# Kernel tuning notes

Hardware: AMD Instinct MI355X
Metric: run time of the kernel (lower is better)

The kernel has to match this reference:

```python
import jax, jax.numpy as jnp
import numpy as np

B, N, D, P_IN, P_OUT = 8, 2048, 32, 8, 4


def setup_inputs() -> dict:
    key = jax.random.key(0)
    k1, k2, k3, k4 = jax.random.split(key, 4)
    U = jax.random.normal(k1, (B, N, D, P_IN), dtype=jnp.float32)
    A = jax.random.uniform(k2, (B, N, N), dtype=jnp.float32)
    W_self = jax.random.normal(k3, (P_IN, P_OUT), dtype=jnp.float32) * 0.01
    W_neigh = jax.random.normal(k4, (P_IN, P_OUT), dtype=jnp.float32) * 0.01
    bias = jnp.zeros((1, 1, 1, P_OUT), dtype=jnp.float32)
    return {"U": U, "A": A, "W_self": W_self, "W_neigh": W_neigh, "bias": bias}


def _stiefel_projection(Y_flat):
    # Polar factor: Y = W S V^T  ->  proj = W V^T (same as Y @ (Y^T Y)^{-1/2})
    u, _, vt = jnp.linalg.svd(Y_flat, full_matrices=False)
    return u @ vt


def reference(U, A, W_self, W_neigh, bias):
    # U: (B,N,d,p_in); A: (B,N,N)
    M_self = jnp.einsum('bndi,io->bndo', U, W_self)
    M_neigh = jnp.einsum('bndi,io->bndo', U, W_neigh)
    # dense neighborhood aggregation: A @ reshape(M_neigh, (B,N,d*p_out))
    M_agg = jnp.einsum('bnm,bmdo->bndo', A, M_neigh)
    Y = jax.nn.relu(M_self + M_agg + bias)
    Y_flat = Y.reshape(B * N, D, P_OUT)
    U_proj = _stiefel_projection(Y_flat)
    return U_proj.reshape(B, N, D, P_OUT)
```

## Files before the change

kernel.cpp:

```cpp
#include <hip/hip_runtime.h>
#include <math.h>

constexpr int B_   = 8;
constexpr int N_   = 2048;
constexpr int D_   = 32;
constexpr int PIN  = 8;
constexpr int POUT = 4;
constexpr int COLS = 128;
constexpr int BM   = 32;
constexpr int BK   = 64;
constexpr int NT   = N_ / BK;

using f32x4  = __attribute__((ext_vector_type(4))) float;
using bf16x8 = __attribute__((ext_vector_type(8))) short;

__device__ __forceinline__ unsigned short f2bf(float f) {
    union { float f; unsigned u; } v; v.f = f;
    unsigned u = v.u + 0x7fffu + ((v.u >> 16) & 1u);
    return (unsigned short)(u >> 16);
}

__global__ __launch_bounds__(256) void mneigh_t_kernel(
    const float* __restrict__ U, const float* __restrict__ Wn,
    unsigned short* __restrict__ Btg)
{
    const int bt = blockIdx.x;
    const int b  = bt >> 5;
    const int n0 = (bt & 31) * 64;
    const int t  = threadIdx.x;
    const int d  = t >> 3;
    const int ns = t & 7;

    float w[PIN][POUT];
#pragma unroll
    for (int p = 0; p < PIN; ++p)
#pragma unroll
        for (int o = 0; o < POUT; ++o) w[p][o] = Wn[p * POUT + o];

    union { unsigned short s[8]; int4 v; } ob[POUT];
    const float* Ub = U + (((size_t)(b * N_ + n0 + ns * 8)) * D_ + d) * PIN;
#pragma unroll
    for (int ni = 0; ni < 8; ++ni) {
        const float4 u0 = *(const float4*)(Ub + (size_t)ni * D_ * PIN);
        const float4 u1 = *(const float4*)(Ub + (size_t)ni * D_ * PIN + 4);
        const float uu[8] = {u0.x, u0.y, u0.z, u0.w, u1.x, u1.y, u1.z, u1.w};
#pragma unroll
        for (int o = 0; o < POUT; ++o) {
            float s = 0.f;
#pragma unroll
            for (int p = 0; p < PIN; ++p) s = fmaf(uu[p], w[p][o], s);
            ob[o].s[ni] = f2bf(s);
        }
    }
#pragma unroll
    for (int o = 0; o < POUT; ++o) {
        unsigned short* dst =
            Btg + ((size_t)(b * COLS + d * 4 + o)) * N_ + n0 + ns * 8;
        *(int4*)dst = ob[o].v;
    }
}

__global__ __launch_bounds__(512) void gemm_proj_kernel(
    const float* __restrict__ A, const unsigned short* __restrict__ Btg,
    const float* __restrict__ U, const float* __restrict__ Wsg,
    const float* __restrict__ bias, float* __restrict__ out)
{
    __shared__ unsigned char smem[40960];
    float* Yl = (float*)smem;
    float* Gp = (float*)(smem + 16896);
    float* Sm = (float*)(smem + 22016);

    const int bid = (blockIdx.x & 7) * 64 + (blockIdx.x >> 3);
    const int b   = bid >> 6;
    const int r0  = (bid & 63) * BM;
    const int t   = threadIdx.x;
    const int lane = t & 63, wv = t >> 6;
    const int wr = wv >> 2, wc = wv & 3;
    const int q = lane >> 4, rl = lane & 15;
    const unsigned swz = (unsigned)((lane & 7) << 4);
    const int rA = wr * 16 + rl;

    const int arow = t >> 4, af4 = t & 15;
    const unsigned aswz = (unsigned)((arow & 7) << 4);
    const int bcol = t >> 2, bsg = t & 3;
    const unsigned bswz = (unsigned)((bcol & 7) << 4);

    const float* Ab = A + (size_t)b * N_ * N_ + (size_t)r0 * N_;
    const unsigned short* Bb = Btg + (size_t)b * COLS * N_;

    f32x4 acc[2] = {f32x4{0, 0, 0, 0}, f32x4{0, 0, 0, 0}};

    {
        const float4 a0 = *(const float4*)(Ab + (size_t)arow * N_ + af4 * 4);
        const int4 b0 = *(const int4*)(Bb + (size_t)bcol * N_ + bsg * 16);
        const int4 b1 = *(const int4*)(Bb + (size_t)bcol * N_ + bsg * 16 + 8);
        union { unsigned short s[4]; int2 v; } pk;
        pk.s[0] = f2bf(a0.x); pk.s[1] = f2bf(a0.y);
        pk.s[2] = f2bf(a0.z); pk.s[3] = f2bf(a0.w);
        *(int2*)(smem + arow * 128 + ((unsigned)(af4 * 8) ^ aswz)) = pk.v;
        *(int4*)(smem + 8192 + bcol * 128 + ((unsigned)(bsg * 32) ^ bswz)) = b0;
        *(int4*)(smem + 8192 + bcol * 128 + ((unsigned)(bsg * 32 + 16) ^ bswz)) = b1;
    }
    __syncthreads();

    for (int kt = 0; kt < NT; ++kt) {
        const unsigned cur = (unsigned)(kt & 1);
        const unsigned nxt = cur ^ 1u;
        float4 na0; int4 nb0, nb1;
        const bool more = (kt + 1 < NT);
        if (more) {
            const int k0 = (kt + 1) * BK;
            na0 = *(const float4*)(Ab + (size_t)arow * N_ + k0 + af4 * 4);
            nb0 = *(const int4*)(Bb + (size_t)bcol * N_ + k0 + bsg * 16);
            nb1 = *(const int4*)(Bb + (size_t)bcol * N_ + k0 + bsg * 16 + 8);
        }
        const unsigned abase = cur * 4096u;
        const unsigned bbase = 8192u + cur * 16384u;
        __builtin_amdgcn_s_setprio(1);
#pragma unroll
        for (int ks = 0; ks < 2; ++ks) {
            const bf16x8 af = *(const bf16x8*)(
                smem + abase + rA * 128 + ((unsigned)(ks * 64 + q * 16) ^ swz));
#pragma unroll
            for (int cf = 0; cf < 2; ++cf) {
                const int rB = wc * 32 + cf * 16 + rl;
                const bf16x8 bfr = *(const bf16x8*)(
                    smem + bbase + rB * 128 + ((unsigned)(ks * 64 + q * 16) ^ swz));
                acc[cf] = __builtin_amdgcn_mfma_f32_16x16x32_bf16(af, bfr, acc[cf],
                                                                  0, 0, 0);
            }
        }
        __builtin_amdgcn_s_setprio(0);
        if (more) {
            union { unsigned short s[4]; int2 v; } pk;
            pk.s[0] = f2bf(na0.x); pk.s[1] = f2bf(na0.y);
            pk.s[2] = f2bf(na0.z); pk.s[3] = f2bf(na0.w);
            *(int2*)(smem + nxt * 4096u + arow * 128 +
                     ((unsigned)(af4 * 8) ^ aswz)) = pk.v;
            *(int4*)(smem + 8192u + nxt * 16384u + bcol * 128 +
                     ((unsigned)(bsg * 32) ^ bswz)) = nb0;
            *(int4*)(smem + 8192u + nxt * 16384u + bcol * 128 +
                     ((unsigned)(bsg * 32 + 16) ^ bswz)) = nb1;
        }
        __syncthreads();
    }

#pragma unroll
    for (int cf = 0; cf < 2; ++cf)
#pragma unroll
        for (int r = 0; r < 4; ++r) {
            const int row = wr * 16 + q * 4 + r;
            const int col = wc * 32 + cf * 16 + rl;
            Yl[row * 132 + col] = acc[cf][r];
        }
    __syncthreads();

    float ws[PIN][POUT];
#pragma unroll
    for (int p = 0; p < PIN; ++p)
#pragma unroll
        for (int o = 0; o < POUT; ++o) ws[p][o] = Wsg[p * POUT + o];
    const float bz[4] = {bias[0], bias[1], bias[2], bias[3]};
#pragma unroll
    for (int i = 0; i < 2; ++i) {
        const int cell = t + i * 512;
        const int row = cell >> 5, d = cell & 31;
        const float* up = U + (((size_t)(b * N_ + r0 + row)) * D_ + d) * PIN;
        const float4 u0 = *(const float4*)up;
        const float4 u1 = *(const float4*)(up + 4);
        const float uu[8] = {u0.x, u0.y, u0.z, u0.w, u1.x, u1.y, u1.z, u1.w};
#pragma unroll
        for (int o = 0; o < POUT; ++o) {
            float s = bz[o];
#pragma unroll
            for (int p = 0; p < PIN; ++p) s = fmaf(uu[p], ws[p][o], s);
            const int idx = row * 132 + d * 4 + o;
            Yl[idx] = fmaxf(Yl[idx] + s, 0.f);
        }
    }
    __syncthreads();

    if (t < 128) {
        const int row = t >> 2, qd = t & 3;
        float g[10] = {0,0,0,0,0,0,0,0,0,0};
#pragma unroll
        for (int d = qd * 8; d < qd * 8 + 8; ++d) {
            const float4 y = *(const float4*)(Yl + row * 132 + 4 * d);
            g[0] = fmaf(y.x, y.x, g[0]); g[1] = fmaf(y.x, y.y, g[1]);
            g[2] = fmaf(y.x, y.z, g[2]); g[3] = fmaf(y.x, y.w, g[3]);
            g[4] = fmaf(y.y, y.y, g[4]); g[5] = fmaf(y.y, y.z, g[5]);
            g[6] = fmaf(y.y, y.w, g[6]); g[7] = fmaf(y.z, y.z, g[7]);
            g[8] = fmaf(y.z, y.w, g[8]); g[9] = fmaf(y.w, y.w, g[9]);
        }
        float* gp = Gp + (row * 4 + qd) * 10;
#pragma unroll
        for (int k = 0; k < 10; ++k) gp[k] = g[k];
    }
    __syncthreads();

    if (t < 32) {
        float gg[10];
#pragma unroll
        for (int k = 0; k < 10; ++k)
            gg[k] = Gp[(t * 4 + 0) * 10 + k] + Gp[(t * 4 + 1) * 10 + k] +
                    Gp[(t * 4 + 2) * 10 + k] + Gp[(t * 4 + 3) * 10 + k];
        float m[4][4] = {{gg[0], gg[1], gg[2], gg[3]},
                         {gg[1], gg[4], gg[5], gg[6]},
                         {gg[2], gg[5], gg[7], gg[8]},
                         {gg[3], gg[6], gg[8], gg[9]}};
        float v[4][4] = {{1,0,0,0},{0,1,0,0},{0,0,1,0},{0,0,0,1}};
        for (int sweep = 0; sweep < 6; ++sweep) {
#pragma unroll
            for (int p = 0; p < 3; ++p) {
#pragma unroll
                for (int qq = p + 1; qq < 4; ++qq) {
                    const float apq = m[p][qq];
                    if (fabsf(apq) < 1e-28f) continue;
                    const float theta = (m[qq][qq] - m[p][p]) / (2.f * apq);
                    const float tt = copysignf(1.f, theta) /
                        (fabsf(theta) + sqrtf(fmaf(theta, theta, 1.f)));
                    const float c = 1.f / sqrtf(fmaf(tt, tt, 1.f));
                    const float s = tt * c;
#pragma unroll
                    for (int k = 0; k < 4; ++k) {
                        const float mkp = m[k][p], mkq = m[k][qq];
                        m[k][p] = c * mkp - s * mkq;
                        m[k][qq] = s * mkp + c * mkq;
                    }
#pragma unroll
                    for (int k = 0; k < 4; ++k) {
                        const float mpk = m[p][k], mqk = m[qq][k];
                        m[p][k] = c * mpk - s * mqk;
                        m[qq][k] = s * mpk + c * mqk;
                    }
#pragma unroll
                    for (int k = 0; k < 4; ++k) {
                        const float vkp = v[k][p], vkq = v[k][qq];
                        v[k][p] = c * vkp - s * vkq;
                        v[k][qq] = s * vkp + c * vkq;
                    }
                }
            }
        }
        const float lam[4] = {m[0][0], m[1][1], m[2][2], m[3][3]};
        const float lmax = fmaxf(fmaxf(lam[0], lam[1]), fmaxf(lam[2], lam[3]));
        const float lfloor = fmaxf(lmax * 1e-12f, 1e-30f);
        float rlv[4];
#pragma unroll
        for (int k = 0; k < 4; ++k) rlv[k] = 1.f / sqrtf(fmaxf(lam[k], lfloor));
#pragma unroll
        for (int i = 0; i < 4; ++i)
#pragma unroll
            for (int j = 0; j < 4; ++j)
                Sm[t * 16 + i * 4 + j] =
                    v[i][0] * v[j][0] * rlv[0] + v[i][1] * v[j][1] * rlv[1] +
                    v[i][2] * v[j][2] * rlv[2] + v[i][3] * v[j][3] * rlv[3];
    }
    __syncthreads();

#pragma unroll
    for (int i = 0; i < 2; ++i) {
        const int cell = t + i * 512;
        const int row = cell >> 5, d = cell & 31;
        const float4 y = *(const float4*)(Yl + row * 132 + 4 * d);
        const float* S = Sm + row * 16;
        float4 o4;
        o4.x = y.x * S[0]  + y.y * S[4]  + y.z * S[8]  + y.w * S[12];
        o4.y = y.x * S[1]  + y.y * S[5]  + y.z * S[9]  + y.w * S[13];
        o4.z = y.x * S[2]  + y.y * S[6]  + y.z * S[10] + y.w * S[14];
        o4.w = y.x * S[3]  + y.y * S[7]  + y.z * S[11] + y.w * S[15];
        *(float4*)(out + ((size_t)(b * N_ + r0 + row)) * COLS + 4 * d) = o4;
    }
}

extern "C" void kernel_launch(void* const* d_in, const int* in_sizes, int n_in,
                              void* d_out, int out_size, void* d_ws, size_t ws_size,
                              hipStream_t stream)
{
    const float* U      = (const float*)d_in[0];
    const float* A      = (const float*)d_in[1];
    const float* Wself  = (const float*)d_in[2];
    const float* Wneigh = (const float*)d_in[3];
    const float* bias   = (const float*)d_in[4];
    float* out = (float*)d_out;

    unsigned short* Btg = (unsigned short*)d_ws;

    mneigh_t_kernel<<<B_ * (N_ / 64), 256, 0, stream>>>(U, Wneigh, Btg);
    gemm_proj_kernel<<<B_ * (N_ / BM), 512, 0, stream>>>(A, Btg, U, Wself, bias,
                                                         out);
}
```

Baseline: 48.60 us.

## Prefetch two K-tiles ahead in GEMM and precompute M_self in the first kernel

The GEMM main loop now keeps two register sets of global loads in flight, issuing loads for tile k+2 while computing tile k. It also replaces __syncthreads with an explicit lgkmcnt wait plus barrier, which should let global loads stay outstanding across the barrier. Separately, the U·W_self product moves into the first kernel and is written to the workspace in fp32, so the epilogue reads a precomputed float4 instead of recomputing from U. In exchange the code uses more registers and adds an extra fp32 workspace write and read. For the last two tiles, the k+2 loads fall back to redundant loads from offset 0.

```diff
diff --git a/kernel.cpp b/kernel.cpp
--- a/kernel.cpp
+++ b/kernel.cpp
@@ -22,7 +22,8 @@
 
 __global__ __launch_bounds__(256) void mneigh_t_kernel(
     const float* __restrict__ U, const float* __restrict__ Wn,
-    unsigned short* __restrict__ Btg)
+    const float* __restrict__ Ws, unsigned short* __restrict__ Btg,
+    float* __restrict__ Mself)
 {
     const int bt = blockIdx.x;
     const int b  = bt >> 5;
@@ -31,11 +32,14 @@
     const int d  = t >> 3;
     const int ns = t & 7;
 
-    float w[PIN][POUT];
+    float wn[PIN][POUT], ws[PIN][POUT];
 #pragma unroll
     for (int p = 0; p < PIN; ++p)
 #pragma unroll
-        for (int o = 0; o < POUT; ++o) w[p][o] = Wn[p * POUT + o];
+        for (int o = 0; o < POUT; ++o) {
+            wn[p][o] = Wn[p * POUT + o];
+            ws[p][o] = Ws[p * POUT + o];
+        }
 
     union { unsigned short s[8]; int4 v; } ob[POUT];
     const float* Ub = U + (((size_t)(b * N_ + n0 + ns * 8)) * D_ + d) * PIN;
@@ -44,13 +48,19 @@
         const float4 u0 = *(const float4*)(Ub + (size_t)ni * D_ * PIN);
         const float4 u1 = *(const float4*)(Ub + (size_t)ni * D_ * PIN + 4);
         const float uu[8] = {u0.x, u0.y, u0.z, u0.w, u1.x, u1.y, u1.z, u1.w};
+        float4 ms;
 #pragma unroll
         for (int o = 0; o < POUT; ++o) {
-            float s = 0.f;
-#pragma unroll
-            for (int p = 0; p < PIN; ++p) s = fmaf(uu[p], w[p][o], s);
-            ob[o].s[ni] = f2bf(s);
-        }
+            float sn = 0.f, ss = 0.f;
+#pragma unroll
+            for (int p = 0; p < PIN; ++p) {
+                sn = fmaf(uu[p], wn[p][o], sn);
+                ss = fmaf(uu[p], ws[p][o], ss);
+            }
+            ob[o].s[ni] = f2bf(sn);
+            ((float*)&ms)[o] = ss;
+        }
+        *(float4*)(Mself + ((size_t)(b * N_ + n0 + ns * 8 + ni)) * COLS + d * 4) = ms;
     }
 #pragma unroll
     for (int o = 0; o < POUT; ++o) {
@@ -62,8 +72,8 @@
 
 __global__ __launch_bounds__(512) void gemm_proj_kernel(
     const float* __restrict__ A, const unsigned short* __restrict__ Btg,
-    const float* __restrict__ U, const float* __restrict__ Wsg,
-    const float* __restrict__ bias, float* __restrict__ out)
+    const float* __restrict__ Mself, const float* __restrict__ bias,
+    float* __restrict__ out)
 {
     __shared__ unsigned char smem[40960];
     float* Yl = (float*)smem;
@@ -90,60 +100,71 @@
 
     f32x4 acc[2] = {f32x4{0, 0, 0, 0}, f32x4{0, 0, 0, 0}};
 
+    float4 A0, A1; int4 B00, B01, B10, B11;
+    A0  = *(const float4*)(Ab + (size_t)arow * N_ + af4 * 4);
+    B00 = *(const int4*)(Bb + (size_t)bcol * N_ + bsg * 16);
+    B01 = *(const int4*)(Bb + (size_t)bcol * N_ + bsg * 16 + 8);
+    A1  = *(const float4*)(Ab + (size_t)arow * N_ + BK + af4 * 4);
+    B10 = *(const int4*)(Bb + (size_t)bcol * N_ + BK + bsg * 16);
+    B11 = *(const int4*)(Bb + (size_t)bcol * N_ + BK + bsg * 16 + 8);
     {
-        const float4 a0 = *(const float4*)(Ab + (size_t)arow * N_ + af4 * 4);
-        const int4 b0 = *(const int4*)(Bb + (size_t)bcol * N_ + bsg * 16);
-        const int4 b1 = *(const int4*)(Bb + (size_t)bcol * N_ + bsg * 16 + 8);
         union { unsigned short s[4]; int2 v; } pk;
-        pk.s[0] = f2bf(a0.x); pk.s[1] = f2bf(a0.y);
-        pk.s[2] = f2bf(a0.z); pk.s[3] = f2bf(a0.w);
+        pk.s[0] = f2bf(A0.x); pk.s[1] = f2bf(A0.y);
+        pk.s[2] = f2bf(A0.z); pk.s[3] = f2bf(A0.w);
         *(int2*)(smem + arow * 128 + ((unsigned)(af4 * 8) ^ aswz)) = pk.v;
-        *(int4*)(smem + 8192 + bcol * 128 + ((unsigned)(bsg * 32) ^ bswz)) = b0;
-        *(int4*)(smem + 8192 + bcol * 128 + ((unsigned)(bsg * 32 + 16) ^ bswz)) = b1;
-    }
-    __syncthreads();
-
-    for (int kt = 0; kt < NT; ++kt) {
-        const unsigned cur = (unsigned)(kt & 1);
-        const unsigned nxt = cur ^ 1u;
-        float4 na0; int4 nb0, nb1;
-        const bool more = (kt + 1 < NT);
-        if (more) {
-            const int k0 = (kt + 1) * BK;
-            na0 = *(const float4*)(Ab + (size_t)arow * N_ + k0 + af4 * 4);
-            nb0 = *(const int4*)(Bb + (size_t)bcol * N_ + k0 + bsg * 16);
-            nb1 = *(const int4*)(Bb + (size_t)bcol * N_ + k0 + bsg * 16 + 8);
-        }
-        const unsigned abase = cur * 4096u;
-        const unsigned bbase = 8192u + cur * 16384u;
-        __builtin_amdgcn_s_setprio(1);
-#pragma unroll
-        for (int ks = 0; ks < 2; ++ks) {
-            const bf16x8 af = *(const bf16x8*)(
-                smem + abase + rA * 128 + ((unsigned)(ks * 64 + q * 16) ^ swz));
-#pragma unroll
-            for (int cf = 0; cf < 2; ++cf) {
-                const int rB = wc * 32 + cf * 16 + rl;
-                const bf16x8 bfr = *(const bf16x8*)(
-                    smem + bbase + rB * 128 + ((unsigned)(ks * 64 + q * 16) ^ swz));
-                acc[cf] = __builtin_amdgcn_mfma_f32_16x16x32_bf16(af, bfr, acc[cf],
-                                                                  0, 0, 0);
-            }
-        }
-        __builtin_amdgcn_s_setprio(0);
-        if (more) {
-            union { unsigned short s[4]; int2 v; } pk;
-            pk.s[0] = f2bf(na0.x); pk.s[1] = f2bf(na0.y);
-            pk.s[2] = f2bf(na0.z); pk.s[3] = f2bf(na0.w);
-            *(int2*)(smem + nxt * 4096u + arow * 128 +
-                     ((unsigned)(af4 * 8) ^ aswz)) = pk.v;
-            *(int4*)(smem + 8192u + nxt * 16384u + bcol * 128 +
-                     ((unsigned)(bsg * 32) ^ bswz)) = nb0;
-            *(int4*)(smem + 8192u + nxt * 16384u + bcol * 128 +
-                     ((unsigned)(bsg * 32 + 16) ^ bswz)) = nb1;
-        }
-        __syncthreads();
-    }
+        *(int4*)(smem + 8192 + bcol * 128 + ((unsigned)(bsg * 32) ^ bswz)) = B00;
+        *(int4*)(smem + 8192 + bcol * 128 + ((unsigned)(bsg * 32 + 16) ^ bswz)) = B01;
+    }
+    asm volatile("s_waitcnt lgkmcnt(0)" ::: "memory");
+    __builtin_amdgcn_s_barrier();
+
+#define PIPE_STEP(KT, RA_, RB0_, RB1_, WA_, WB0_, WB1_, CUR)                     \
+    {                                                                            \
+        const int k2 = ((KT) + 2 < NT) ? ((KT) + 2) * BK : 0;                    \
+        RA_  = *(const float4*)(Ab + (size_t)arow * N_ + k2 + af4 * 4);          \
+        RB0_ = *(const int4*)(Bb + (size_t)bcol * N_ + k2 + bsg * 16);           \
+        RB1_ = *(const int4*)(Bb + (size_t)bcol * N_ + k2 + bsg * 16 + 8);       \
+        const unsigned abase = (CUR) * 4096u;                                    \
+        const unsigned bbase = 8192u + (CUR) * 16384u;                           \
+        __builtin_amdgcn_s_setprio(1);                                           \
+        _Pragma("unroll")                                                        \
+        for (int ks = 0; ks < 2; ++ks) {                                         \
+            const bf16x8 af = *(const bf16x8*)(                                  \
+                smem + abase + rA * 128 + ((unsigned)(ks * 64 + q * 16) ^ swz)); \
+            _Pragma("unroll")                                                    \
+            for (int cf = 0; cf < 2; ++cf) {                                     \
+                const int rB = wc * 32 + cf * 16 + rl;                           \
+                const bf16x8 bfr = *(const bf16x8*)(                             \
+                    smem + bbase + rB * 128 +                                    \
+                    ((unsigned)(ks * 64 + q * 16) ^ swz));                       \
+                acc[cf] = __builtin_amdgcn_mfma_f32_16x16x32_bf16(               \
+                    af, bfr, acc[cf], 0, 0, 0);                                  \
+            }                                                                    \
+        }                                                                        \
+        __builtin_amdgcn_s_setprio(0);                                           \
+        {                                                                        \
+            union { unsigned short s[4]; int2 v; } pk;                           \
+            pk.s[0] = f2bf(WA_.x); pk.s[1] = f2bf(WA_.y);                        \
+            pk.s[2] = f2bf(WA_.z); pk.s[3] = f2bf(WA_.w);                        \
+            const unsigned nab = ((CUR) ^ 1u) * 4096u;                           \
+            const unsigned nbb = 8192u + ((CUR) ^ 1u) * 16384u;                  \
+            *(int2*)(smem + nab + arow * 128 +                                   \
+                     ((unsigned)(af4 * 8) ^ aswz)) = pk.v;                       \
+            *(int4*)(smem + nbb + bcol * 128 +                                   \
+                     ((unsigned)(bsg * 32) ^ bswz)) = WB0_;                      \
+            *(int4*)(smem + nbb + bcol * 128 +                                   \
+                     ((unsigned)(bsg * 32 + 16) ^ bswz)) = WB1_;                 \
+        }                                                                        \
+        asm volatile("s_waitcnt lgkmcnt(0)" ::: "memory");                       \
+        __builtin_amdgcn_s_barrier();                                            \
+    }
+
+    for (int kt = 0; kt < NT; kt += 2) {
+        PIPE_STEP(kt,     A0, B00, B01, A1, B10, B11, 0u)
+        PIPE_STEP(kt + 1, A1, B10, B11, A0, B00, B01, 1u)
+    }
+#undef PIPE_STEP
+    __syncthreads();
 
 #pragma unroll
     for (int cf = 0; cf < 2; ++cf)
@@ -155,28 +176,20 @@
         }
     __syncthreads();
 
-    float ws[PIN][POUT];
-#pragma unroll
-    for (int p = 0; p < PIN; ++p)
-#pragma unroll
-        for (int o = 0; o < POUT; ++o) ws[p][o] = Wsg[p * POUT + o];
     const float bz[4] = {bias[0], bias[1], bias[2], bias[3]};
+    const float* Mb = Mself + ((size_t)(b * N_ + r0)) * COLS;
 #pragma unroll
     for (int i = 0; i < 2; ++i) {
         const int cell = t + i * 512;
         const int row = cell >> 5, d = cell & 31;
-        const float* up = U + (((size_t)(b * N_ + r0 + row)) * D_ + d) * PIN;
-        const float4 u0 = *(const float4*)up;
-        const float4 u1 = *(const float4*)(up + 4);
-        const float uu[8] = {u0.x, u0.y, u0.z, u0.w, u1.x, u1.y, u1.z, u1.w};
-#pragma unroll
-        for (int o = 0; o < POUT; ++o) {
-            float s = bz[o];
-#pragma unroll
-            for (int p = 0; p < PIN; ++p) s = fmaf(uu[p], ws[p][o], s);
-            const int idx = row * 132 + d * 4 + o;
-            Yl[idx] = fmaxf(Yl[idx] + s, 0.f);
-        }
+        const float4 m = *(const float4*)(Mb + (size_t)row * COLS + d * 4);
+        const int idx = row * 132 + d * 4;
+        float4 y = *(const float4*)(Yl + idx);
+        y.x = fmaxf(y.x + m.x + bz[0], 0.f);
+        y.y = fmaxf(y.y + m.y + bz[1], 0.f);
+        y.z = fmaxf(y.z + m.z + bz[2], 0.f);
+        y.w = fmaxf(y.w + m.w + bz[3], 0.f);
+        *(float4*)(Yl + idx) = y;
     }
     __syncthreads();
 
@@ -285,8 +298,10 @@
     float* out = (float*)d_out;
 
     unsigned short* Btg = (unsigned short*)d_ws;
-
-    mneigh_t_kernel<<<B_ * (N_ / 64), 256, 0, stream>>>(U, Wneigh, Btg);
-    gemm_proj_kernel<<<B_ * (N_ / BM), 512, 0, stream>>>(A, Btg, U, Wself, bias,
+    float* Mself = (float*)((char*)d_ws + (size_t)B_ * COLS * N_ * 2);
+
+    mneigh_t_kernel<<<B_ * (N_ / 64), 256, 0, stream>>>(U, Wneigh, Wself, Btg,
+                                                        Mself);
+    gemm_proj_kernel<<<B_ * (N_ / BM), 512, 0, stream>>>(A, Btg, Mself, bias,
                                                          out);
 }
```

Result: no change. 49.32 us (+1.5%).
